# Optimization experiments

Hardware: AMD Instinct MI355X
Metric: run time of the kernel (lower is better)

## Reference

```python
import jax, jax.numpy as jnp
import numpy as np

GROUP_SIZE = 64
OUT_F, IN_F = 11008, 4096
W_SHAPE = (OUT_F, IN_F)


def quantize_q40(w):
    # w: fp32 weight, numel divisible by GROUP_SIZE
    wg = w.reshape(-1, GROUP_SIZE)                      # [N, G]
    wmax = jnp.max(jnp.abs(wg), axis=1)
    scale = (wmax / 7.0).astype(jnp.float16)[:, None]   # [N, 1] fp16 per-group scale
    quant = wg / scale.astype(jnp.float32)
    q = jnp.round(quant).astype(jnp.int8)               # values in [-7, 7]
    pairs = q.reshape(-1, 2, GROUP_SIZE)                # even rows -> MSB nibble, odd -> LSB
    packed = ((pairs[:, 0] << 4) | (pairs[:, 1] & 15)).astype(jnp.int8)  # [N/2, G]
    return packed, scale


def dequantize_q40(w, scale):
    # w: int8 packed [N/2, G]; arithmetic shifts sign-extend each nibble
    msb = w >> 4
    lsb = (w << 4) >> 4
    full = jnp.concatenate([msb, lsb], axis=1).reshape(-1, GROUP_SIZE)  # interleave back to [N, G]
    return (full.astype(jnp.float16) * scale).reshape(W_SHAPE)


def setup_inputs() -> dict:
    key = jax.random.key(0)
    kx, kw = jax.random.split(key)
    x = jax.random.normal(kx, (4, 2048, IN_F), dtype=jnp.float16)
    w_fp = jax.random.normal(kw, W_SHAPE, dtype=jnp.float32) * 0.02
    linear_w, linear_s = quantize_q40(w_fp)
    return {"x": x, "linear_w": linear_w, "linear_s": linear_s}


def reference(x, linear_w, linear_s):
    # dequantize packed int4 weights to fp16, then dense linear (no bias)
    deq = dequantize_q40(linear_w, linear_s)            # [OUT_F, IN_F] fp16
    return jnp.einsum('bsi,oi->bso', x, deq)            # F.linear(x, deq)
```

## Files before the change

### kernel.cpp

```cpp
#include <hip/hip_runtime.h>
#include <stdint.h>

#define IN_F   4096
#define OUT_F  11008
#define M_ROWS 8192
#define BM 256
#define BN 256
#define BK 64
#define NTILE_K (IN_F / BK)

typedef __attribute__((ext_vector_type(4))) float  f32x4;
typedef __attribute__((ext_vector_type(4))) int    int4v;
typedef __attribute__((ext_vector_type(8))) unsigned short ushort8;
typedef __bf16 bf16x8 __attribute__((ext_vector_type(8)));

__device__ __forceinline__ unsigned short f2bf(float f) {
  unsigned int u = __builtin_bit_cast(unsigned int, f);
  u += 0x7fffu + ((u >> 16) & 1u);
  return (unsigned short)(u >> 16);
}

__global__ __launch_bounds__(256) void dequant_q40(const int* __restrict__ w,
                                                   const float* __restrict__ sc,
                                                   unsigned short* __restrict__ wb) {
  const int total8 = (OUT_F * IN_F) / 8;
  for (int t = blockIdx.x * blockDim.x + threadIdx.x; t < total8;
       t += gridDim.x * blockDim.x) {
    const int f0  = t * 8;
    const int p   = f0 >> 7;
    const int nib = (f0 >> 6) & 1;
    const int j0  = f0 & 63;
    const float scale = sc[f0 >> 6];
    const int* src = w + p * 64 + j0;
    const int4v b0 = *reinterpret_cast<const int4v*>(src);
    const int4v b1 = *reinterpret_cast<const int4v*>(src + 4);
    ushort8 r;
#pragma unroll
    for (int e = 0; e < 4; ++e) {
      const int v0 = b0[e], v1 = b1[e];
      const int q0 = nib ? ((v0 << 28) >> 28) : (v0 >> 4);
      const int q1 = nib ? ((v1 << 28) >> 28) : (v1 >> 4);
      r[e]     = f2bf((float)q0 * scale);
      r[4 + e] = f2bf((float)q1 * scale);
    }
    *reinterpret_cast<ushort8*>(wb + f0) = r;
  }
}

__global__ __launch_bounds__(256) void cvt_x(const float* __restrict__ x,
                                             unsigned short* __restrict__ xb) {
  const int total8 = (M_ROWS * IN_F) / 8;
  for (int t = blockIdx.x * blockDim.x + threadIdx.x; t < total8;
       t += gridDim.x * blockDim.x) {
    const f32x4 a0 = *reinterpret_cast<const f32x4*>(x + t * 8);
    const f32x4 a1 = *reinterpret_cast<const f32x4*>(x + t * 8 + 4);
    ushort8 r;
#pragma unroll
    for (int e = 0; e < 4; ++e) {
      r[e]     = f2bf(a0[e]);
      r[4 + e] = f2bf(a1[e]);
    }
    *reinterpret_cast<ushort8*>(xb + t * 8) = r;
  }
}

__device__ __forceinline__ void gld16(const void* g, void* l) {
  __builtin_amdgcn_global_load_lds(
      (const __attribute__((address_space(1))) unsigned int*)(uintptr_t)g,
      (__attribute__((address_space(3))) unsigned int*)(unsigned int)(uintptr_t)l,
      16, 0, 0);
}

#define BAR() do { asm volatile("" ::: "memory"); __builtin_amdgcn_s_barrier(); \
                   asm volatile("" ::: "memory"); } while (0)

__global__ __launch_bounds__(512, 2) void gemm_bt(const unsigned short* __restrict__ A,
                                                  const unsigned short* __restrict__ B,
                                                  float* __restrict__ C) {
  __shared__ __align__(16) unsigned short lds[65536];

  const int NT  = OUT_F / BN;
  const int nwg = (M_ROWS / BM) * NT;
  const int cpx = nwg >> 3;
  const int bid = blockIdx.x;
  const int swz = (bid & 7) * cpx + (bid >> 3);
  const int mt  = swz / NT;
  const int nt  = swz - mt * NT;

  const int tid  = threadIdx.x;
  const int lane = tid & 63;
  const int wid  = tid >> 6;
  const int wr   = wid >> 2;
  const int wc   = wid & 3;

  const int p_row   = tid >> 3;
  const int l_chunk = (tid & 7) ^ (p_row & 7);
  const unsigned short* gA = A + (size_t)(mt * BM + p_row) * IN_F + l_chunk * 8;
  const unsigned short* gB = B + (size_t)(nt * BM + p_row) * IN_F + l_chunk * 8;
  unsigned short* ldsw = lds + tid * 8;

#define STAGE_A(p, c, kk) gld16(gA + (size_t)(64 * (c)) * IN_F + (kk), \
                                ldsw + (p) * 32768 + (c) * 4096)
#define STAGE_B(p, c, kk) gld16(gB + (size_t)(64 * (c)) * IN_F + (kk), \
                                ldsw + (p) * 32768 + 16384 + (c) * 4096)

  const int fr   = lane & 15;
  const int kq   = lane >> 4;
  const int axor = lane & 7;
  const int c0   = ((kq) ^ axor) * 8;
  const int c1   = ((4 + kq) ^ axor) * 8;
#define RD(base, row)
#define RDF(base, row, cs) (*reinterpret_cast<const bf16x8*>((base) + (size_t)(row) * 64 + (cs)))

  f32x4 acc[8][4] = {};
  bf16x8 a[4][2], b[4][2];

#define MFMA_Q(mh, nh) do {                                                        \
    __builtin_amdgcn_s_setprio(1);                                                 \
    _Pragma("unroll") for (int mm = 0; mm < 4; ++mm)                               \
      _Pragma("unroll") for (int nn = 0; nn < 2; ++nn) {                           \
        acc[(mh)*4+mm][(nh)*2+nn] = __builtin_amdgcn_mfma_f32_16x16x32_bf16(       \
            a[mm][0], b[(nh)*2+nn][0], acc[(mh)*4+mm][(nh)*2+nn], 0, 0, 0);        \
        acc[(mh)*4+mm][(nh)*2+nn] = __builtin_amdgcn_mfma_f32_16x16x32_bf16(       \
            a[mm][1], b[(nh)*2+nn][1], acc[(mh)*4+mm][(nh)*2+nn], 0, 0, 0);        \
      }                                                                            \
    __builtin_amdgcn_s_setprio(0);                                                 \
  } while (0)

  STAGE_A(0, 0, 0); STAGE_A(0, 1, 0); STAGE_A(0, 2, 0); STAGE_A(0, 3, 0);
  STAGE_B(0, 0, 0); STAGE_B(0, 1, 0); STAGE_B(0, 2, 0); STAGE_B(0, 3, 0);
  STAGE_A(1, 0, BK); STAGE_A(1, 1, BK); STAGE_A(1, 2, BK); STAGE_A(1, 3, BK);
  asm volatile("s_waitcnt vmcnt(4)" ::: "memory");
  __builtin_amdgcn_s_barrier();
  asm volatile("" ::: "memory");

  for (int t = 0; t < NTILE_K; ++t) {
    const int p = t & 1, q = p ^ 1;
    const unsigned short* bufA = lds + p * 32768;
    const unsigned short* bufB = bufA + 16384;
    const int k1 = (t + 1 < NTILE_K ? t + 1 : 0) * BK;
    const int k2 = (t + 2 < NTILE_K ? t + 2 : t + 2 - NTILE_K) * BK;

#pragma unroll
    for (int m = 0; m < 4; ++m) {
      const int r = wr * 128 + m * 16 + fr;
      a[m][0] = RDF(bufA, r, c0); a[m][1] = RDF(bufA, r, c1);
    }
#pragma unroll
    for (int n = 0; n < 4; ++n) {
      const int r = wc * 64 + n * 16 + fr;
      b[n][0] = RDF(bufB, r, c0); b[n][1] = RDF(bufB, r, c1);
    }
    STAGE_B(q, 0, k1); STAGE_B(q, 1, k1);
    BAR();
    MFMA_Q(0, 0);
    BAR();

    STAGE_B(q, 2, k1); STAGE_B(q, 3, k1);
    BAR();
    MFMA_Q(0, 1);
    BAR();

#pragma unroll
    for (int m = 0; m < 4; ++m) {
      const int r = wr * 128 + 64 + m * 16 + fr;
      a[m][0] = RDF(bufA, r, c0); a[m][1] = RDF(bufA, r, c1);
    }
    BAR();
    MFMA_Q(1, 1);
    BAR();

    STAGE_A(p, 0, k2); STAGE_A(p, 1, k2); STAGE_A(p, 2, k2); STAGE_A(p, 3, k2);
    asm volatile("s_waitcnt vmcnt(4)" ::: "memory");
    BAR();
    MFMA_Q(1, 0);
    BAR();
  }

  const int col  = nt * BN + wc * 64 + fr;
  const int row0 = mt * BM + wr * 128 + (lane >> 4) * 4;
#pragma unroll
  for (int m = 0; m < 8; ++m) {
    const int ro = (m >> 2) * 64 + (m & 3) * 16;
#pragma unroll
    for (int n = 0; n < 4; ++n) {
      float* cp = C + (size_t)(row0 + ro) * OUT_F + (col + n * 16);
#pragma unroll
      for (int r = 0; r < 4; ++r) cp[(size_t)r * OUT_F] = acc[m][n][r];
    }
  }
}

extern "C" void kernel_launch(void* const* d_in, const int* in_sizes, int n_in,
                              void* d_out, int out_size, void* d_ws, size_t ws_size,
                              hipStream_t stream) {
  const float* x = (const float*)d_in[0];
  const int*   w = (const int*)d_in[1];
  const float* s = (const float*)d_in[2];
  float*     out = (float*)d_out;

  unsigned short* wb = (unsigned short*)d_ws;
  unsigned short* xb = wb + (size_t)OUT_F * IN_F;

  dequant_q40<<<dim3(2048), dim3(256), 0, stream>>>(w, s, wb);
  cvt_x<<<dim3(2048), dim3(256), 0, stream>>>(x, xb);
  gemm_bt<<<dim3((M_ROWS / BM) * (OUT_F / BN)), dim3(512), 0, stream>>>(xb, wb, out);
}
```

Baseline: 755.0 us.

## Restructure GEMM main loop into four A-quarter segments with interleaved LDS reads

Rewrites the K-loop schedule so each wave walks its A rows in four 32-row segments. A fragments are double-buffered in registers (sA/sBst), so LDS reads for the next segment overlap the MFMAs of the current one. All global-to-LDS loads for the next tile now go to the other buffer, with prefetch depth one tile instead of the previous A two-ahead scheme. The next tile's B reads are interleaved into the final segment's MFMAs. Sched_barriers pin the ordering. This trades deeper A prefetch and some extra waits for better LDS/MFMA overlap and fewer register fragments live at once.

```diff
diff --git a/kernel.cpp b/kernel.cpp
--- a/kernel.cpp
+++ b/kernel.cpp
@@ -71,8 +71,9 @@
       16, 0, 0);
 }
 
-#define BAR() do { asm volatile("" ::: "memory"); __builtin_amdgcn_s_barrier(); \
-                   asm volatile("" ::: "memory"); } while (0)
+#define BARRIER() do { asm volatile("" ::: "memory"); __builtin_amdgcn_s_barrier(); \
+                       asm volatile("" ::: "memory"); } while (0)
+#define SCHEDB()  __builtin_amdgcn_sched_barrier(0)
 
 __global__ __launch_bounds__(512, 2) void gemm_bt(const unsigned short* __restrict__ A,
                                                   const unsigned short* __restrict__ B,
@@ -109,82 +110,100 @@
   const int axor = lane & 7;
   const int c0   = ((kq) ^ axor) * 8;
   const int c1   = ((4 + kq) ^ axor) * 8;
-#define RD(base, row)
 #define RDF(base, row, cs) (*reinterpret_cast<const bf16x8*>((base) + (size_t)(row) * 64 + (cs)))
 
+#define RD_A(dst, buf, mq) do {                                          \
+    _Pragma("unroll") for (int mm = 0; mm < 2; ++mm) {                   \
+      const int r_ = wr * 128 + (mq) * 32 + mm * 16 + fr;                \
+      dst[mm][0] = RDF(buf, r_, c0); dst[mm][1] = RDF(buf, r_, c1);      \
+    } } while (0)
+
   f32x4 acc[8][4] = {};
-  bf16x8 a[4][2], b[4][2];
-
-#define MFMA_Q(mh, nh) do {                                                        \
+  bf16x8 sA[2][2], sBst[2][2], b[4][2];
+
+#define MFMA_SEG(mi, aset) do {                                                    \
     __builtin_amdgcn_s_setprio(1);                                                 \
-    _Pragma("unroll") for (int mm = 0; mm < 4; ++mm)                               \
-      _Pragma("unroll") for (int nn = 0; nn < 2; ++nn) {                           \
-        acc[(mh)*4+mm][(nh)*2+nn] = __builtin_amdgcn_mfma_f32_16x16x32_bf16(       \
-            a[mm][0], b[(nh)*2+nn][0], acc[(mh)*4+mm][(nh)*2+nn], 0, 0, 0);        \
-        acc[(mh)*4+mm][(nh)*2+nn] = __builtin_amdgcn_mfma_f32_16x16x32_bf16(       \
-            a[mm][1], b[(nh)*2+nn][1], acc[(mh)*4+mm][(nh)*2+nn], 0, 0, 0);        \
+    _Pragma("unroll") for (int mm = 0; mm < 2; ++mm)                               \
+      _Pragma("unroll") for (int nn = 0; nn < 4; ++nn) {                           \
+        acc[(mi)*2+mm][nn] = __builtin_amdgcn_mfma_f32_16x16x32_bf16(              \
+            aset[mm][0], b[nn][0], acc[(mi)*2+mm][nn], 0, 0, 0);                   \
+        acc[(mi)*2+mm][nn] = __builtin_amdgcn_mfma_f32_16x16x32_bf16(              \
+            aset[mm][1], b[nn][1], acc[(mi)*2+mm][nn], 0, 0, 0);                   \
       }                                                                            \
     __builtin_amdgcn_s_setprio(0);                                                 \
   } while (0)
 
   STAGE_A(0, 0, 0); STAGE_A(0, 1, 0); STAGE_A(0, 2, 0); STAGE_A(0, 3, 0);
   STAGE_B(0, 0, 0); STAGE_B(0, 1, 0); STAGE_B(0, 2, 0); STAGE_B(0, 3, 0);
-  STAGE_A(1, 0, BK); STAGE_A(1, 1, BK); STAGE_A(1, 2, BK); STAGE_A(1, 3, BK);
-  asm volatile("s_waitcnt vmcnt(4)" ::: "memory");
+  asm volatile("s_waitcnt vmcnt(0)" ::: "memory");
   __builtin_amdgcn_s_barrier();
   asm volatile("" ::: "memory");
+  {
+    const unsigned short* bufB0 = lds + 16384;
+#pragma unroll
+    for (int nn = 0; nn < 4; ++nn) {
+      const int rb = wc * 64 + nn * 16 + fr;
+      b[nn][0] = RDF(bufB0, rb, c0); b[nn][1] = RDF(bufB0, rb, c1);
+    }
+    RD_A(sA, lds, 0);
+  }
 
   for (int t = 0; t < NTILE_K; ++t) {
     const int p = t & 1, q = p ^ 1;
-    const unsigned short* bufA = lds + p * 32768;
-    const unsigned short* bufB = bufA + 16384;
+    const unsigned short* bufAp = lds + p * 32768;
+    const unsigned short* bufAq = lds + q * 32768;
+    const unsigned short* bufBq = bufAq + 16384;
     const int k1 = (t + 1 < NTILE_K ? t + 1 : 0) * BK;
-    const int k2 = (t + 2 < NTILE_K ? t + 2 : t + 2 - NTILE_K) * BK;
-
-#pragma unroll
-    for (int m = 0; m < 4; ++m) {
-      const int r = wr * 128 + m * 16 + fr;
-      a[m][0] = RDF(bufA, r, c0); a[m][1] = RDF(bufA, r, c1);
-    }
-#pragma unroll
-    for (int n = 0; n < 4; ++n) {
-      const int r = wc * 64 + n * 16 + fr;
-      b[n][0] = RDF(bufB, r, c0); b[n][1] = RDF(bufB, r, c1);
-    }
-    STAGE_B(q, 0, k1); STAGE_B(q, 1, k1);
-    BAR();
-    MFMA_Q(0, 0);
-    BAR();
-
-    STAGE_B(q, 2, k1); STAGE_B(q, 3, k1);
-    BAR();
-    MFMA_Q(0, 1);
-    BAR();
-
-#pragma unroll
-    for (int m = 0; m < 4; ++m) {
-      const int r = wr * 128 + 64 + m * 16 + fr;
-      a[m][0] = RDF(bufA, r, c0); a[m][1] = RDF(bufA, r, c1);
-    }
-    BAR();
-    MFMA_Q(1, 1);
-    BAR();
-
-    STAGE_A(p, 0, k2); STAGE_A(p, 1, k2); STAGE_A(p, 2, k2); STAGE_A(p, 3, k2);
-    asm volatile("s_waitcnt vmcnt(4)" ::: "memory");
-    BAR();
-    MFMA_Q(1, 0);
-    BAR();
+
+    RD_A(sBst, bufAp, 1);
+    STAGE_B(q, 0, k1); STAGE_B(q, 1, k1); STAGE_B(q, 2, k1); STAGE_B(q, 3, k1);
+    STAGE_A(q, 0, k1); STAGE_A(q, 2, k1);
+    BARRIER(); SCHEDB();
+    MFMA_SEG(0, sA);
+    SCHEDB();
+    asm volatile("s_waitcnt vmcnt(6)" ::: "memory");
+    BARRIER();
+
+    RD_A(sA, bufAp, 2);
+    STAGE_A(q, 1, k1);
+    BARRIER(); SCHEDB();
+    MFMA_SEG(1, sBst);
+    SCHEDB();
+    BARRIER();
+
+    RD_A(sBst, bufAp, 3);
+    STAGE_A(q, 3, k1);
+    BARRIER(); SCHEDB();
+    MFMA_SEG(2, sA);
+    SCHEDB();
+    asm volatile("s_waitcnt vmcnt(2)" ::: "memory");
+    BARRIER();
+
+    RD_A(sA, bufAq, 0);
+    BARRIER(); SCHEDB();
+    __builtin_amdgcn_s_setprio(1);
+#pragma unroll
+    for (int nn = 0; nn < 4; ++nn) {
+      acc[6][nn] = __builtin_amdgcn_mfma_f32_16x16x32_bf16(sBst[0][0], b[nn][0], acc[6][nn], 0, 0, 0);
+      acc[6][nn] = __builtin_amdgcn_mfma_f32_16x16x32_bf16(sBst[0][1], b[nn][1], acc[6][nn], 0, 0, 0);
+      acc[7][nn] = __builtin_amdgcn_mfma_f32_16x16x32_bf16(sBst[1][0], b[nn][0], acc[7][nn], 0, 0, 0);
+      acc[7][nn] = __builtin_amdgcn_mfma_f32_16x16x32_bf16(sBst[1][1], b[nn][1], acc[7][nn], 0, 0, 0);
+      const int rb = wc * 64 + nn * 16 + fr;
+      b[nn][0] = RDF(bufBq, rb, c0);
+      b[nn][1] = RDF(bufBq, rb, c1);
+    }
+    __builtin_amdgcn_s_setprio(0);
+    SCHEDB();
+    BARRIER();
   }
 
   const int col  = nt * BN + wc * 64 + fr;
   const int row0 = mt * BM + wr * 128 + (lane >> 4) * 4;
 #pragma unroll
   for (int m = 0; m < 8; ++m) {
-    const int ro = (m >> 2) * 64 + (m & 3) * 16;
 #pragma unroll
     for (int n = 0; n < 4; ++n) {
-      float* cp = C + (size_t)(row0 + ro) * OUT_F + (col + n * 16);
+      float* cp = C + (size_t)(row0 + m * 16) * OUT_F + (col + n * 16);
 #pragma unroll
       for (int r = 0; r < 4; ++r) cp[(size_t)r * OUT_F] = acc[m][n][r];
     }
```

Measured after the change: 760.8 us. No clear change (+0.8%).
